# Optimization experiments

Hardware: AMD Instinct MI355X
Metric: run time of the kernel (lower is better)

## Reference

```python
import jax, jax.numpy as jnp
import numpy as np

N = 100000   # nodes
F = 256      # in_dim
D = 128      # out_dim
K = 2        # hops (K+1 adjacency matrices)
E = 1600000  # edges per hop (avg degree 16)


def setup_inputs() -> dict:
    key = jax.random.key(0)
    ks = jax.random.split(key, 8)
    node_features = jax.random.normal(ks[0], (N, F), dtype=jnp.float32)
    edge_rows = jax.random.randint(ks[1], (K + 1, E), 0, N, dtype=jnp.int32)
    edge_cols = jax.random.randint(ks[2], (K + 1, E), 0, N, dtype=jnp.int32)
    edge_vals = jax.random.uniform(ks[3], (K + 1, E), dtype=jnp.float32)
    W_embed = jax.random.normal(ks[4], (F, D), dtype=jnp.float32) / np.sqrt(F)
    W_feat = jax.random.normal(ks[5], (K + 1, F, D), dtype=jnp.float32) / np.sqrt(F)
    W_embK = jax.random.normal(ks[6], (K + 1, D, D), dtype=jnp.float32) / np.sqrt(D)
    alpha = jnp.asarray(0.1, dtype=jnp.float32)  # learnable scalar, clipped to [0,1]
    return {
        'node_features': node_features,
        'edge_rows': edge_rows,
        'edge_cols': edge_cols,
        'edge_vals': edge_vals,
        'W_embed': W_embed,
        'W_feat': W_feat,
        'W_embK': W_embK,
        'alpha': alpha,
    }


def reference(node_features, edge_rows, edge_cols, edge_vals, W_embed, W_feat, W_embK, alpha):
    # learned_embeddings = Dense(out_dim, no bias)(X)  -> [N, D]
    learned = node_features @ W_embed
    out = jnp.zeros((node_features.shape[0], W_embed.shape[1]), dtype=node_features.dtype)
    for hop in range(K + 1):
        # feature projection for this hop: [N, D]
        fw = node_features @ W_feat[hop]
        # SpMM: A_hop @ fw via COO gather + scatter-add
        msgs = edge_vals[hop][:, None] * fw[edge_cols[hop]]            # [E, D]
        structural = jax.ops.segment_sum(msgs, edge_rows[hop], num_segments=node_features.shape[0])
        learned_h = learned @ W_embK[hop]                              # [N, D]
        out = out + structural + alpha * learned_h
    # dropout is identity at inference (training=False)
    return jax.nn.relu(out)
```

## Files before the change

kernel.cpp:

```cpp
#include <hip/hip_runtime.h>
#include <hip/hip_bf16.h>

#define F_DIM 256
#define D_DIM 128
#define NHOPS 3
#define KPB   1000
#define NBMAX 512

using short8 = __attribute__((ext_vector_type(8))) short;
using f32x4  = __attribute__((ext_vector_type(4))) float;

static __device__ __forceinline__ unsigned short f2bf(float f) {
    unsigned int u = __float_as_uint(f);
    unsigned int r = (u + 0x7fffu + ((u >> 16) & 1u)) >> 16;
    return (unsigned short)r;
}
static __device__ __forceinline__ float bf2f(unsigned short b) {
    return __uint_as_float(((unsigned int)b) << 16);
}

__global__ void wsum_kernel(const float* __restrict__ W_embK,
                            const float* __restrict__ alpha,
                            float* __restrict__ Wsum) {
    int i = blockIdx.x * blockDim.x + threadIdx.x;
    if (i < D_DIM * D_DIM) {
        float a = alpha[0];
        Wsum[i] = a * (W_embK[i] + W_embK[D_DIM * D_DIM + i] + W_embK[2 * D_DIM * D_DIM + i]);
    }
}

__global__ void wc_kernel(const float* __restrict__ W_embed,
                          const float* __restrict__ Wsum,
                          float* __restrict__ Wc) {
    int i = blockIdx.x * blockDim.x + threadIdx.x;
    if (i < F_DIM * D_DIM) {
        int f = i / D_DIM, d = i % D_DIM;
        float acc = 0.f;
        #pragma unroll 8
        for (int k = 0; k < D_DIM; ++k)
            acc = fmaf(W_embed[f * D_DIM + k], Wsum[k * D_DIM + d], acc);
        Wc[i] = acc;
    }
}

__global__ void pack_wt(const float* __restrict__ Wc,
                        const float* __restrict__ W_feat,
                        unsigned short* __restrict__ Wt) {
    int i = blockIdx.x * blockDim.x + threadIdx.x;
    int j = i >> 8, k = i & 255;
    float v = (j < 128)
        ? Wc[k * D_DIM + j]
        : W_feat[(size_t)((j - 128) >> 7) * F_DIM * D_DIM + k * D_DIM + ((j - 128) & 127)];
    Wt[i] = f2bf(v);
}

__global__ void xcast_kernel(const float* __restrict__ X, unsigned short* __restrict__ Xb,
                             int n4) {
    int i = blockIdx.x * blockDim.x + threadIdx.x;
    int stride = gridDim.x * blockDim.x;
    for (; i < n4; i += stride) {
        float4 v = ((const float4*)X)[i];
        ushort4 p;
        p.x = f2bf(v.x); p.y = f2bf(v.y); p.z = f2bf(v.z); p.w = f2bf(v.w);
        ((ushort4*)Xb)[i] = p;
    }
}


__global__ __launch_bounds__(256) void bhist_kernel(const int* __restrict__ rows,
                                                    int* __restrict__ bcount,
                                                    int N, int E, int TE) {
    __shared__ int h[NBMAX];
    int tid = threadIdx.x;
    for (int i = tid; i < NBMAX; i += 256) h[i] = 0;
    __syncthreads();
    int c0 = blockIdx.x * 4096;
    #pragma unroll
    for (int i = 0; i < 16; ++i) {
        int ge = c0 + tid + i * 256;
        if (ge < TE) {
            int row = rows[ge];
            int hp = (ge >= E) + (ge >= 2 * E);
            int key = hp * N + row;
            atomicAdd(&h[key / KPB], 1);
        }
    }
    __syncthreads();
    for (int b = tid; b < NBMAX; b += 256)
        if (h[b]) atomicAdd(&bcount[b], h[b]);
}

__global__ void bscan_kernel(const int* __restrict__ bcount, int* __restrict__ bstart,
                             int* __restrict__ gcur, int NB) {
    __shared__ int s[NBMAX + 1];
    int tid = threadIdx.x;
    for (int i = tid; i < NB; i += 256) s[i] = bcount[i];
    __syncthreads();
    if (tid == 0) {
        int run = 0;
        for (int i = 0; i < NB; ++i) { int c = s[i]; s[i] = run; run += c; }
        s[NB] = run;
    }
    __syncthreads();
    for (int i = tid; i <= NB; i += 256) {
        bstart[i] = s[i];
        if (i < NB) gcur[i] = s[i];
    }
}

__global__ __launch_bounds__(256) void bucket_scatter(const int* __restrict__ rows,
                                                      const int* __restrict__ cols,
                                                      const float* __restrict__ vals,
                                                      int* __restrict__ gcur,
                                                      int2* __restrict__ cvb,
                                                      int N, int E, int TE) {
    __shared__ int sh_hist[NBMAX];
    __shared__ int sh_gof[NBMAX];
    int tid = threadIdx.x;
    for (int i = tid; i < NBMAX; i += 256) sh_hist[i] = 0;
    __syncthreads();
    int c0 = blockIdx.x * 4096;
    unsigned meta[16];
    #pragma unroll
    for (int i = 0; i < 16; ++i) {
        int ge = c0 + tid + i * 256;
        unsigned m = 0;
        if (ge < TE) {
            int row = rows[ge];
            int hp = (ge >= E) + (ge >= 2 * E);
            int key = hp * N + row;
            int b = key / KPB;
            int lkey = key - b * KPB;
            int rank = atomicAdd(&sh_hist[b], 1);
            m = ((unsigned)lkey << 22) | ((unsigned)b << 13) | (unsigned)rank;
        }
        meta[i] = m;
    }
    __syncthreads();
    for (int b = tid; b < NBMAX; b += 256)
        if (sh_hist[b]) sh_gof[b] = atomicAdd(&gcur[b], sh_hist[b]);
    __syncthreads();
    #pragma unroll
    for (int i = 0; i < 16; ++i) {
        int ge = c0 + tid + i * 256;
        if (ge < TE) {
            unsigned m = meta[i];
            int rank = m & 8191;
            int b = (m >> 13) & 511;
            int lkey = m >> 22;
            int col = cols[ge];
            float v = vals[ge];
            cvb[sh_gof[b] + rank] = make_int2(col | (lkey << 17), __float_as_int(v));
        }
    }
}

__global__ __launch_bounds__(256) void local_sort(const int2* __restrict__ cvb,
                                                  const int* __restrict__ bstart,
                                                  int2* __restrict__ cv,
                                                  int* __restrict__ offsets,
                                                  int M, int TE, int NB) {
    __shared__ int h[1024];
    __shared__ int part[256];
    const int tid = threadIdx.x;
    const int b = blockIdx.x;
    const int s = bstart[b], e = bstart[b + 1];

    for (int k = tid; k < 1024; k += 256) h[k] = 0;
    __syncthreads();
    for (int i = s + tid; i < e; i += 256) {
        unsigned lkey = ((unsigned)cvb[i].x) >> 17;
        atomicAdd(&h[lkey], 1);
    }
    __syncthreads();
    int base4 = tid * 4;
    int a0 = h[base4], a1 = h[base4 + 1], a2 = h[base4 + 2], a3 = h[base4 + 3];
    part[tid] = a0 + a1 + a2 + a3;
    __syncthreads();
    for (int off = 1; off < 256; off <<= 1) {
        int t = (tid >= off) ? part[tid - off] : 0;
        __syncthreads();
        part[tid] += t;
        __syncthreads();
    }
    int pbase = tid ? part[tid - 1] : 0;
    h[base4]     = pbase;
    h[base4 + 1] = pbase + a0;
    h[base4 + 2] = pbase + a0 + a1;
    h[base4 + 3] = pbase + a0 + a1 + a2;
    __syncthreads();
    for (int k = tid; k < KPB; k += 256) {
        int key = b * KPB + k;
        if (key < M) offsets[key] = s + h[k];
    }
    if (b == NB - 1 && tid == 0) offsets[M] = TE;
    __syncthreads();
    for (int i = s + tid; i < e; i += 256) {
        int2 rec = cvb[i];
        unsigned lkey = ((unsigned)rec.x) >> 17;
        int p = s + atomicAdd(&h[lkey], 1);
        cv[p] = make_int2(rec.x & 0x1FFFF, rec.y);
    }
}


__global__ void hist_kernel(const int* __restrict__ rows, int* __restrict__ counts,
                            int N, int E) {
    int idx = blockIdx.x * blockDim.x + threadIdx.x;
    int h = blockIdx.y;
    if (idx < E) atomicAdd(&counts[h * N + rows[(size_t)h * E + idx]], 1);
}

__global__ void scan1(const int* __restrict__ counts, int* __restrict__ tmp,
                      int* __restrict__ bsums, int M) {
    __shared__ int s[256];
    int tid = threadIdx.x, i = blockIdx.x * 256 + tid;
    int v = (i < M) ? counts[i] : 0;
    s[tid] = v; __syncthreads();
    for (int off = 1; off < 256; off <<= 1) {
        int t = (tid >= off) ? s[tid - off] : 0;
        __syncthreads();
        s[tid] += t;
        __syncthreads();
    }
    if (i < M) tmp[i] = s[tid] - v;
    if (tid == 255) bsums[blockIdx.x] = s[255];
}

__global__ void scan2(int* __restrict__ bsums, int nb) {
    __shared__ int s[256];
    int tid = threadIdx.x;
    int carry = 0;
    for (int base = 0; base < nb; base += 256) {
        int v = (base + tid < nb) ? bsums[base + tid] : 0;
        s[tid] = v; __syncthreads();
        for (int off = 1; off < 256; off <<= 1) {
            int t = (tid >= off) ? s[tid - off] : 0;
            __syncthreads();
            s[tid] += t;
            __syncthreads();
        }
        if (base + tid < nb) bsums[base + tid] = carry + s[tid] - v;
        carry += s[255];
        __syncthreads();
    }
}

__global__ void scan3(int* __restrict__ tmp, const int* __restrict__ bsums,
                      int* __restrict__ offsets, int M, int total) {
    int i = blockIdx.x * blockDim.x + threadIdx.x;
    if (i < M) {
        int e = tmp[i] + bsums[i >> 8];
        offsets[i] = e;
        tmp[i] = e;
    }
    if (i == 0) offsets[M] = total;
}

__global__ void scatter_kernel(const int* __restrict__ rows, const int* __restrict__ cols,
                               const float* __restrict__ vals, int* __restrict__ cursors,
                               int2* __restrict__ cv, int N, int E) {
    int idx = blockIdx.x * blockDim.x + threadIdx.x;
    int h = blockIdx.y;
    if (idx < E) {
        size_t e = (size_t)h * E + idx;
        int r = rows[e];
        int p = atomicAdd(&cursors[h * N + r], 1);
        cv[p] = make_int2(cols[e], __float_as_int(vals[e]));
    }
}

template <bool BF16A>
__global__ __launch_bounds__(256) void gemm_mfma(const float* __restrict__ X,
                                                 const unsigned short* __restrict__ Xb,
                                                 const unsigned short* __restrict__ Wt,
                                                 float* __restrict__ out,
                                                 unsigned short* __restrict__ fw,
                                                 int N) {
    __shared__ __align__(16) unsigned short As[128][40];
    __shared__ __align__(16) unsigned short Bs[128][40];

    const int tid = threadIdx.x;
    const int w = tid >> 6, lane = tid & 63;
    const int bm = blockIdx.x, bn = blockIdx.y;
    const int row0 = bm * 128;
    const int wm = (w & 1) * 64, wn = (w >> 1) * 64;
    const int l15 = lane & 15, lk = (lane >> 4) * 8;

    f32x4 acc[4][4] = {};

    for (int k0 = 0; k0 < F_DIM; k0 += 32) {
        float4 bv[2];
        #pragma unroll
        for (int i = 0; i < 2; ++i) {
            int idx = tid + i * 256;
            int br = idx >> 2, kq = (idx & 3) << 3;
            bv[i] = *(const float4*)&Wt[((size_t)(bn * 128 + br)) * F_DIM + k0 + kq];
        }
        if constexpr (BF16A) {
            short8 av[2];
            #pragma unroll
            for (int i = 0; i < 2; ++i) {
                int idx = tid + i * 256;
                int ar = idx >> 2, kq = (idx & 3) << 3;
                int gr = row0 + ar; if (gr >= N) gr = N - 1;
                av[i] = *(const short8*)&Xb[(size_t)gr * F_DIM + k0 + kq];
            }
            __syncthreads();
            #pragma unroll
            for (int i = 0; i < 2; ++i) {
                int idx = tid + i * 256;
                int ar = idx >> 2, kq = (idx & 3) << 3;
                *(short8*)&As[ar][kq] = av[i];
            }
        } else {
            float4 av[4];
            #pragma unroll
            for (int i = 0; i < 4; ++i) {
                int idx = tid + i * 256;
                int ar = idx >> 3, kq = (idx & 7) << 2;
                int gr = row0 + ar; if (gr >= N) gr = N - 1;
                av[i] = *(const float4*)&X[(size_t)gr * F_DIM + k0 + kq];
            }
            __syncthreads();
            #pragma unroll
            for (int i = 0; i < 4; ++i) {
                int idx = tid + i * 256;
                int ar = idx >> 3, kq = (idx & 7) << 2;
                ushort4 p;
                p.x = f2bf(av[i].x); p.y = f2bf(av[i].y);
                p.z = f2bf(av[i].z); p.w = f2bf(av[i].w);
                *(ushort4*)&As[ar][kq] = p;
            }
        }
        #pragma unroll
        for (int i = 0; i < 2; ++i) {
            int idx = tid + i * 256;
            int br = idx >> 2, kq = (idx & 3) << 3;
            *(float4*)&Bs[br][kq] = bv[i];
        }
        __syncthreads();

        short8 af[4], bfr[4];
        #pragma unroll
        for (int mi = 0; mi < 4; ++mi) af[mi]  = *(const short8*)&As[wm + mi * 16 + l15][lk];
        #pragma unroll
        for (int ni = 0; ni < 4; ++ni) bfr[ni] = *(const short8*)&Bs[wn + ni * 16 + l15][lk];
        #pragma unroll
        for (int mi = 0; mi < 4; ++mi)
            #pragma unroll
            for (int ni = 0; ni < 4; ++ni)
                acc[mi][ni] = __builtin_amdgcn_mfma_f32_16x16x32_bf16(af[mi], bfr[ni], acc[mi][ni], 0, 0, 0);
        __syncthreads();
    }

    if (bn == 0) {
        #pragma unroll
        for (int mi = 0; mi < 4; ++mi) {
            int rowb = row0 + wm + mi * 16 + (lane >> 4) * 4;
            #pragma unroll
            for (int ni = 0; ni < 4; ++ni) {
                int col = wn + ni * 16 + l15;
                #pragma unroll
                for (int j = 0; j < 4; ++j) {
                    int rr = rowb + j;
                    if (rr < N) out[(size_t)rr * D_DIM + col] = acc[mi][ni][j];
                }
            }
        }
    } else {
        unsigned short* dst = fw + (size_t)(bn - 1) * N * D_DIM;
        #pragma unroll
        for (int mi = 0; mi < 4; ++mi) {
            int rowb = row0 + wm + mi * 16 + (lane >> 4) * 4;
            #pragma unroll
            for (int ni = 0; ni < 4; ++ni) {
                int col = wn + ni * 16 + l15;
                #pragma unroll
                for (int j = 0; j < 4; ++j) {
                    int rr = rowb + j;
                    if (rr < N) dst[(size_t)rr * D_DIM + col] = f2bf(acc[mi][ni][j]);
                }
            }
        }
    }
}

__global__ __launch_bounds__(256) void spmm_csr(const int* __restrict__ off,
                                                const int2* __restrict__ cv,
                                                const unsigned short* __restrict__ fw,
                                                float* __restrict__ out, int N) {
    const int w = threadIdx.x >> 6, lane = threadIdx.x & 63;
    const int r = blockIdx.x * 4 + w;
    if (r >= N) return;
    const int sub = lane >> 4;
    const int dp  = lane & 15;
    const size_t obase = (size_t)r * D_DIM + dp * 8;

    float acc[8];
    if (sub == 0) {
        float4 a = *(const float4*)&out[obase];
        float4 b = *(const float4*)&out[obase + 4];
        acc[0] = a.x; acc[1] = a.y; acc[2] = a.z; acc[3] = a.w;
        acc[4] = b.x; acc[5] = b.y; acc[6] = b.z; acc[7] = b.w;
    } else {
        #pragma unroll
        for (int j = 0; j < 8; ++j) acc[j] = 0.f;
    }

    #pragma unroll
    for (int h = 0; h < NHOPS; ++h) {
        const unsigned short* fwh = fw + (size_t)h * N * D_DIM;
        int s = off[h * N + r], e = off[h * N + r + 1];
        int i = s + sub;
        for (; i + 4 < e; i += 8) {
            int2 ca = cv[i];
            int2 cb = cv[i + 4];
            short8 pa = *(const short8*)&fwh[(size_t)ca.x * D_DIM + dp * 8];
            short8 pb = *(const short8*)&fwh[(size_t)cb.x * D_DIM + dp * 8];
            float va = __int_as_float(ca.y);
            float vb = __int_as_float(cb.y);
            #pragma unroll
            for (int j = 0; j < 8; ++j)
                acc[j] = fmaf(va, bf2f((unsigned short)pa[j]), acc[j]);
            #pragma unroll
            for (int j = 0; j < 8; ++j)
                acc[j] = fmaf(vb, bf2f((unsigned short)pb[j]), acc[j]);
        }
        if (i < e) {
            int2 ca = cv[i];
            short8 pa = *(const short8*)&fwh[(size_t)ca.x * D_DIM + dp * 8];
            float va = __int_as_float(ca.y);
            #pragma unroll
            for (int j = 0; j < 8; ++j)
                acc[j] = fmaf(va, bf2f((unsigned short)pa[j]), acc[j]);
        }
    }

    #pragma unroll
    for (int j = 0; j < 8; ++j) {
        acc[j] += __shfl_xor(acc[j], 16, 64);
        acc[j] += __shfl_xor(acc[j], 32, 64);
    }

    if (sub == 0) {
        float4 a = {fmaxf(acc[0], 0.f), fmaxf(acc[1], 0.f), fmaxf(acc[2], 0.f), fmaxf(acc[3], 0.f)};
        float4 b = {fmaxf(acc[4], 0.f), fmaxf(acc[5], 0.f), fmaxf(acc[6], 0.f), fmaxf(acc[7], 0.f)};
        *(float4*)&out[obase]     = a;
        *(float4*)&out[obase + 4] = b;
    }
}

extern "C" void kernel_launch(void* const* d_in, const int* in_sizes, int n_in,
                              void* d_out, int out_size, void* d_ws, size_t ws_size,
                              hipStream_t stream) {
    const float* X         = (const float*)d_in[0];
    const int*   edge_rows = (const int*)d_in[1];
    const int*   edge_cols = (const int*)d_in[2];
    const float* edge_vals = (const float*)d_in[3];
    const float* W_embed   = (const float*)d_in[4];
    const float* W_feat    = (const float*)d_in[5];
    const float* W_embK    = (const float*)d_in[6];
    const float* alpha     = (const float*)d_in[7];
    float* out = (float*)d_out;

    const int N  = in_sizes[0] / F_DIM;
    const int E  = in_sizes[1] / NHOPS;
    const int M  = NHOPS * N;
    const int TE = NHOPS * E;
    const int NB = (M + KPB - 1) / KPB;

    auto al = [](size_t x) { return (x + 255) & ~(size_t)255; };
    const size_t sz_cv   = al((size_t)TE * 8);
    const size_t sz_fwb  = al((size_t)M * D_DIM * 2);
    const size_t sz_xb   = al((size_t)N * F_DIM * 2);
    const size_t sz_off  = al((size_t)(M + 1) * 4);
    const size_t sz_m    = al((size_t)M * 4);
    const size_t sz_b    = al((size_t)(NBMAX + 1) * 4);
    const size_t sz_w    = al(D_DIM * D_DIM * 4) + al(F_DIM * D_DIM * 4) + al(512 * F_DIM * 2);
    const size_t need_mid = 2 * sz_cv + sz_fwb + sz_off + 3 * sz_b + sz_w;
    const size_t need_big = need_mid + sz_xb;

    const bool ok_new = (NB <= NBMAX) && (N < (1 << 17));
    const int mode = (ok_new && ws_size >= need_big) ? 2
                   : (ok_new && ws_size >= need_mid) ? 1 : 0;

    char* wsb = (char*)d_ws;
    size_t o = 0;
    auto take = [&](size_t bytes) -> char* {
        char* p = wsb + o;
        o += al(bytes);
        return p;
    };

    if (mode >= 1) {
        int2*           cvb     = (int2*)take((size_t)TE * 8);
        int2*           cv      = (int2*)take((size_t)TE * 8);
        unsigned short* fwb     = (unsigned short*)take((size_t)M * D_DIM * 2);
        int*            offsets = (int*)take((size_t)(M + 1) * 4);
        int*            bcount  = (int*)take((NBMAX + 1) * 4);
        int*            bstart  = (int*)take((NBMAX + 1) * 4);
        int*            gcur    = (int*)take((NBMAX + 1) * 4);
        float*          Wsum    = (float*)take(D_DIM * D_DIM * 4);
        float*          Wc      = (float*)take(F_DIM * D_DIM * 4);
        unsigned short* Wt      = (unsigned short*)take(512 * F_DIM * 2);
        unsigned short* Xb      = (mode == 2) ? (unsigned short*)take((size_t)N * F_DIM * 2) : nullptr;

        const int nchunk = (TE + 4095) / 4096;
        hipMemsetAsync(bcount, 0, NBMAX * 4, stream);
        bhist_kernel<<<nchunk, 256, 0, stream>>>(edge_rows, bcount, N, E, TE);
        bscan_kernel<<<1, 256, 0, stream>>>(bcount, bstart, gcur, NB);
        bucket_scatter<<<nchunk, 256, 0, stream>>>(edge_rows, edge_cols, edge_vals,
                                                   gcur, cvb, N, E, TE);
        local_sort<<<NB, 256, 0, stream>>>(cvb, bstart, cv, offsets, M, TE, NB);

        wsum_kernel<<<(D_DIM * D_DIM + 255) / 256, 256, 0, stream>>>(W_embK, alpha, Wsum);
        wc_kernel<<<(F_DIM * D_DIM + 255) / 256, 256, 0, stream>>>(W_embed, Wsum, Wc);
        pack_wt<<<(512 * F_DIM) / 256, 256, 0, stream>>>(Wc, W_feat, Wt);

        dim3 g((N + 127) / 128, 4);
        if (mode == 2) {
            xcast_kernel<<<2048, 256, 0, stream>>>(X, Xb, N * F_DIM / 4);
            gemm_mfma<true><<<g, 256, 0, stream>>>(X, Xb, Wt, out, fwb, N);
        } else {
            gemm_mfma<false><<<g, 256, 0, stream>>>(X, nullptr, Wt, out, fwb, N);
        }

        spmm_csr<<<(N + 3) / 4, 256, 0, stream>>>(offsets, cv, fwb, out, N);
    } else {
        int2*           cv      = (int2*)take((size_t)TE * 8);
        unsigned short* fwb     = (unsigned short*)take((size_t)M * D_DIM * 2);
        int*            counts  = (int*)take((size_t)M * 4);
        int*            cursors = (int*)take((size_t)M * 4);
        int*            offsets = (int*)take((size_t)(M + 1) * 4);
        int*            bsums   = (int*)take(8192);
        float*          Wsum    = (float*)take(D_DIM * D_DIM * 4);
        float*          Wc      = (float*)take(F_DIM * D_DIM * 4);
        unsigned short* Wt      = (unsigned short*)take(512 * F_DIM * 2);

        hipMemsetAsync(counts, 0, (size_t)M * 4, stream);
        dim3 ge((E + 255) / 256, NHOPS);
        hist_kernel<<<ge, 256, 0, stream>>>(edge_rows, counts, N, E);
        int nb = (M + 255) / 256;
        scan1<<<nb, 256, 0, stream>>>(counts, cursors, bsums, M);
        scan2<<<1, 256, 0, stream>>>(bsums, nb);
        scan3<<<nb, 256, 0, stream>>>(cursors, bsums, offsets, M, TE);
        scatter_kernel<<<ge, 256, 0, stream>>>(edge_rows, edge_cols, edge_vals,
                                               cursors, cv, N, E);

        wsum_kernel<<<(D_DIM * D_DIM + 255) / 256, 256, 0, stream>>>(W_embK, alpha, Wsum);
        wc_kernel<<<(F_DIM * D_DIM + 255) / 256, 256, 0, stream>>>(W_embed, Wsum, Wc);
        pack_wt<<<(512 * F_DIM) / 256, 256, 0, stream>>>(Wc, W_feat, Wt);

        dim3 g((N + 127) / 128, 4);
        gemm_mfma<false><<<g, 256, 0, stream>>>(X, nullptr, Wt, out, fwb, N);

        spmm_csr<<<(N + 3) / 4, 256, 0, stream>>>(offsets, cv, fwb, out, N);
    }
}
```

Baseline: 662.2 us.

## Shrink sort buckets to 256 keys, fuse weight packing, unroll SpMM with nontemporal loads

Bucket size drops from 1000 to 256 keys so bucket and local-key math uses shifts, and the local sort needs a single 256-entry histogram and scan. The bucket scan becomes a parallel chunked scan, since the bucket count grows to about 1200. The two weight-prep kernels are merged into one pack_all kernel that caches a Wsum column in shared memory. The SpMM inner loop is unrolled to four edges per step and reads cv with nontemporal loads. The main risk is that the rank field now has 12 bits, so a bucket with more than 4096 entries in one chunk would overflow, though that is unlikely here.

```diff
diff --git a/kernel.cpp b/kernel.cpp
--- a/kernel.cpp
+++ b/kernel.cpp
@@ -4,8 +4,8 @@
 #define F_DIM 256
 #define D_DIM 128
 #define NHOPS 3
-#define KPB   1000
-#define NBMAX 512
+#define KPB   256
+#define NBMAX 2048
 
 using short8 = __attribute__((ext_vector_type(8))) short;
 using f32x4  = __attribute__((ext_vector_type(4))) float;
@@ -17,6 +17,11 @@
 }
 static __device__ __forceinline__ float bf2f(unsigned short b) {
     return __uint_as_float(((unsigned int)b) << 16);
+}
+static __device__ __forceinline__ int2 ldnt_i2(const int2* p) {
+    long long raw = __builtin_nontemporal_load((const long long*)p);
+    int2 r; r.x = (int)(raw & 0xffffffffLL); r.y = (int)(raw >> 32);
+    return r;
 }
 
 __global__ void wsum_kernel(const float* __restrict__ W_embK,
@@ -29,29 +34,25 @@
     }
 }
 
-__global__ void wc_kernel(const float* __restrict__ W_embed,
-                          const float* __restrict__ Wsum,
-                          float* __restrict__ Wc) {
-    int i = blockIdx.x * blockDim.x + threadIdx.x;
-    if (i < F_DIM * D_DIM) {
-        int f = i / D_DIM, d = i % D_DIM;
+__global__ __launch_bounds__(256) void pack_all(const float* __restrict__ W_embed,
+                                                const float* __restrict__ W_feat,
+                                                const float* __restrict__ Wsum,
+                                                unsigned short* __restrict__ Wt) {
+    __shared__ float wcol[D_DIM];
+    const int j = blockIdx.x;
+    const int k = threadIdx.x;
+    if (j < D_DIM) {
+        for (int i = k; i < D_DIM; i += 256) wcol[i] = Wsum[i * D_DIM + j];
+        __syncthreads();
         float acc = 0.f;
         #pragma unroll 8
-        for (int k = 0; k < D_DIM; ++k)
-            acc = fmaf(W_embed[f * D_DIM + k], Wsum[k * D_DIM + d], acc);
-        Wc[i] = acc;
-    }
-}
-
-__global__ void pack_wt(const float* __restrict__ Wc,
-                        const float* __restrict__ W_feat,
-                        unsigned short* __restrict__ Wt) {
-    int i = blockIdx.x * blockDim.x + threadIdx.x;
-    int j = i >> 8, k = i & 255;
-    float v = (j < 128)
-        ? Wc[k * D_DIM + j]
-        : W_feat[(size_t)((j - 128) >> 7) * F_DIM * D_DIM + k * D_DIM + ((j - 128) & 127)];
-    Wt[i] = f2bf(v);
+        for (int kk = 0; kk < D_DIM; ++kk)
+            acc = fmaf(W_embed[k * D_DIM + kk], wcol[kk], acc);
+        Wt[(size_t)j * F_DIM + k] = f2bf(acc);
+    } else {
+        int hp = (j - D_DIM) >> 7, d = (j - D_DIM) & 127;
+        Wt[(size_t)j * F_DIM + k] = f2bf(W_feat[(size_t)hp * F_DIM * D_DIM + k * D_DIM + d]);
+    }
 }
 
 __global__ void xcast_kernel(const float* __restrict__ X, unsigned short* __restrict__ Xb,
@@ -81,8 +82,7 @@
         if (ge < TE) {
             int row = rows[ge];
             int hp = (ge >= E) + (ge >= 2 * E);
-            int key = hp * N + row;
-            atomicAdd(&h[key / KPB], 1);
+            atomicAdd(&h[(hp * N + row) >> 8], 1);
         }
     }
     __syncthreads();
@@ -90,22 +90,28 @@
         if (h[b]) atomicAdd(&bcount[b], h[b]);
 }
 
-__global__ void bscan_kernel(const int* __restrict__ bcount, int* __restrict__ bstart,
-                             int* __restrict__ gcur, int NB) {
-    __shared__ int s[NBMAX + 1];
+__global__ __launch_bounds__(256) void bscan_kernel(const int* __restrict__ bcount,
+                                                    int* __restrict__ bstart,
+                                                    int* __restrict__ gcur, int NB) {
+    __shared__ int s[256];
     int tid = threadIdx.x;
-    for (int i = tid; i < NB; i += 256) s[i] = bcount[i];
-    __syncthreads();
-    if (tid == 0) {
-        int run = 0;
-        for (int i = 0; i < NB; ++i) { int c = s[i]; s[i] = run; run += c; }
-        s[NB] = run;
-    }
-    __syncthreads();
-    for (int i = tid; i <= NB; i += 256) {
-        bstart[i] = s[i];
-        if (i < NB) gcur[i] = s[i];
-    }
+    int carry = 0;
+    for (int base = 0; base < NB; base += 256) {
+        int idx = base + tid;
+        int v = (idx < NB) ? bcount[idx] : 0;
+        s[tid] = v; __syncthreads();
+        for (int off = 1; off < 256; off <<= 1) {
+            int t = (tid >= off) ? s[tid - off] : 0;
+            __syncthreads();
+            s[tid] += t;
+            __syncthreads();
+        }
+        int excl = carry + s[tid] - v;
+        if (idx < NB) { bstart[idx] = excl; gcur[idx] = excl; }
+        carry += s[255];
+        __syncthreads();
+    }
+    if (tid == 0) bstart[NB] = carry;
 }
 
 __global__ __launch_bounds__(256) void bucket_scatter(const int* __restrict__ rows,
@@ -129,10 +135,10 @@
             int row = rows[ge];
             int hp = (ge >= E) + (ge >= 2 * E);
             int key = hp * N + row;
-            int b = key / KPB;
-            int lkey = key - b * KPB;
+            int b = key >> 8;
+            int lkey = key & 255;
             int rank = atomicAdd(&sh_hist[b], 1);
-            m = ((unsigned)lkey << 22) | ((unsigned)b << 13) | (unsigned)rank;
+            m = ((unsigned)lkey << 23) | ((unsigned)b << 12) | (unsigned)rank;
         }
         meta[i] = m;
     }
@@ -145,12 +151,11 @@
         int ge = c0 + tid + i * 256;
         if (ge < TE) {
             unsigned m = meta[i];
-            int rank = m & 8191;
-            int b = (m >> 13) & 511;
-            int lkey = m >> 22;
-            int col = cols[ge];
-            float v = vals[ge];
-            cvb[sh_gof[b] + rank] = make_int2(col | (lkey << 17), __float_as_int(v));
+            int rank = m & 4095;
+            int b = (m >> 12) & 2047;
+            int lkey = m >> 23;
+            cvb[sh_gof[b] + rank] = make_int2(cols[ge] | (lkey << 17),
+                                              __float_as_int(vals[ge]));
         }
     }
 }
@@ -160,40 +165,30 @@
                                                   int2* __restrict__ cv,
                                                   int* __restrict__ offsets,
                                                   int M, int TE, int NB) {
-    __shared__ int h[1024];
-    __shared__ int part[256];
+    __shared__ int h[256];
+    __shared__ int sc[256];
     const int tid = threadIdx.x;
     const int b = blockIdx.x;
     const int s = bstart[b], e = bstart[b + 1];
 
-    for (int k = tid; k < 1024; k += 256) h[k] = 0;
-    __syncthreads();
-    for (int i = s + tid; i < e; i += 256) {
-        unsigned lkey = ((unsigned)cvb[i].x) >> 17;
-        atomicAdd(&h[lkey], 1);
-    }
-    __syncthreads();
-    int base4 = tid * 4;
-    int a0 = h[base4], a1 = h[base4 + 1], a2 = h[base4 + 2], a3 = h[base4 + 3];
-    part[tid] = a0 + a1 + a2 + a3;
-    __syncthreads();
+    h[tid] = 0;
+    __syncthreads();
+    for (int i = s + tid; i < e; i += 256)
+        atomicAdd(&h[((unsigned)cvb[i].x) >> 17], 1);
+    __syncthreads();
+    int v = h[tid];
+    sc[tid] = v; __syncthreads();
     for (int off = 1; off < 256; off <<= 1) {
-        int t = (tid >= off) ? part[tid - off] : 0;
-        __syncthreads();
-        part[tid] += t;
-        __syncthreads();
-    }
-    int pbase = tid ? part[tid - 1] : 0;
-    h[base4]     = pbase;
-    h[base4 + 1] = pbase + a0;
-    h[base4 + 2] = pbase + a0 + a1;
-    h[base4 + 3] = pbase + a0 + a1 + a2;
-    __syncthreads();
-    for (int k = tid; k < KPB; k += 256) {
-        int key = b * KPB + k;
-        if (key < M) offsets[key] = s + h[k];
-    }
+        int t = (tid >= off) ? sc[tid - off] : 0;
+        __syncthreads();
+        sc[tid] += t;
+        __syncthreads();
+    }
+    int excl = sc[tid] - v;
+    int key = (b << 8) + tid;
+    if (key < M) offsets[key] = s + excl;
     if (b == NB - 1 && tid == 0) offsets[M] = TE;
+    h[tid] = excl;
     __syncthreads();
     for (int i = s + tid; i < e; i += 256) {
         int2 rec = cvb[i];
@@ -413,27 +408,43 @@
         const unsigned short* fwh = fw + (size_t)h * N * D_DIM;
         int s = off[h * N + r], e = off[h * N + r + 1];
         int i = s + sub;
+        for (; i + 12 < e; i += 16) {
+            int2 c0 = ldnt_i2(cv + i);
+            int2 c1 = ldnt_i2(cv + i + 4);
+            int2 c2 = ldnt_i2(cv + i + 8);
+            int2 c3 = ldnt_i2(cv + i + 12);
+            short8 p0 = *(const short8*)&fwh[(size_t)c0.x * D_DIM + dp * 8];
+            short8 p1 = *(const short8*)&fwh[(size_t)c1.x * D_DIM + dp * 8];
+            short8 p2 = *(const short8*)&fwh[(size_t)c2.x * D_DIM + dp * 8];
+            short8 p3 = *(const short8*)&fwh[(size_t)c3.x * D_DIM + dp * 8];
+            float v0 = __int_as_float(c0.y), v1 = __int_as_float(c1.y);
+            float v2 = __int_as_float(c2.y), v3 = __int_as_float(c3.y);
+            #pragma unroll
+            for (int j = 0; j < 8; ++j) acc[j] = fmaf(v0, bf2f((unsigned short)p0[j]), acc[j]);
+            #pragma unroll
+            for (int j = 0; j < 8; ++j) acc[j] = fmaf(v1, bf2f((unsigned short)p1[j]), acc[j]);
+            #pragma unroll
+            for (int j = 0; j < 8; ++j) acc[j] = fmaf(v2, bf2f((unsigned short)p2[j]), acc[j]);
+            #pragma unroll
+            for (int j = 0; j < 8; ++j) acc[j] = fmaf(v3, bf2f((unsigned short)p3[j]), acc[j]);
+        }
         for (; i + 4 < e; i += 8) {
-            int2 ca = cv[i];
-            int2 cb = cv[i + 4];
-            short8 pa = *(const short8*)&fwh[(size_t)ca.x * D_DIM + dp * 8];
-            short8 pb = *(const short8*)&fwh[(size_t)cb.x * D_DIM + dp * 8];
-            float va = __int_as_float(ca.y);
-            float vb = __int_as_float(cb.y);
-            #pragma unroll
-            for (int j = 0; j < 8; ++j)
-                acc[j] = fmaf(va, bf2f((unsigned short)pa[j]), acc[j]);
-            #pragma unroll
-            for (int j = 0; j < 8; ++j)
-                acc[j] = fmaf(vb, bf2f((unsigned short)pb[j]), acc[j]);
+            int2 c0 = ldnt_i2(cv + i);
+            int2 c1 = ldnt_i2(cv + i + 4);
+            short8 p0 = *(const short8*)&fwh[(size_t)c0.x * D_DIM + dp * 8];
+            short8 p1 = *(const short8*)&fwh[(size_t)c1.x * D_DIM + dp * 8];
+            float v0 = __int_as_float(c0.y), v1 = __int_as_float(c1.y);
+            #pragma unroll
+            for (int j = 0; j < 8; ++j) acc[j] = fmaf(v0, bf2f((unsigned short)p0[j]), acc[j]);
+            #pragma unroll
+            for (int j = 0; j < 8; ++j) acc[j] = fmaf(v1, bf2f((unsigned short)p1[j]), acc[j]);
         }
         if (i < e) {
-            int2 ca = cv[i];
-            short8 pa = *(const short8*)&fwh[(size_t)ca.x * D_DIM + dp * 8];
-            float va = __int_as_float(ca.y);
-            #pragma unroll
-            for (int j = 0; j < 8; ++j)
-                acc[j] = fmaf(va, bf2f((unsigned short)pa[j]), acc[j]);
+            int2 c0 = ldnt_i2(cv + i);
+            short8 p0 = *(const short8*)&fwh[(size_t)c0.x * D_DIM + dp * 8];
+            float v0 = __int_as_float(c0.y);
+            #pragma unroll
+            for (int j = 0; j < 8; ++j) acc[j] = fmaf(v0, bf2f((unsigned short)p0[j]), acc[j]);
         }
     }
 
@@ -471,13 +482,12 @@
     const int NB = (M + KPB - 1) / KPB;
 
     auto al = [](size_t x) { return (x + 255) & ~(size_t)255; };
-    const size_t sz_cv   = al((size_t)TE * 8);
-    const size_t sz_fwb  = al((size_t)M * D_DIM * 2);
-    const size_t sz_xb   = al((size_t)N * F_DIM * 2);
-    const size_t sz_off  = al((size_t)(M + 1) * 4);
-    const size_t sz_m    = al((size_t)M * 4);
-    const size_t sz_b    = al((size_t)(NBMAX + 1) * 4);
-    const size_t sz_w    = al(D_DIM * D_DIM * 4) + al(F_DIM * D_DIM * 4) + al(512 * F_DIM * 2);
+    const size_t sz_cv  = al((size_t)TE * 8);
+    const size_t sz_fwb = al((size_t)M * D_DIM * 2);
+    const size_t sz_xb  = al((size_t)N * F_DIM * 2);
+    const size_t sz_off = al((size_t)(M + 1) * 4);
+    const size_t sz_b   = al((size_t)(NBMAX + 1) * 4);
+    const size_t sz_w   = al(D_DIM * D_DIM * 4) + al(512 * F_DIM * 2);
     const size_t need_mid = 2 * sz_cv + sz_fwb + sz_off + 3 * sz_b + sz_w;
     const size_t need_big = need_mid + sz_xb;
 
@@ -502,7 +512,6 @@
         int*            bstart  = (int*)take((NBMAX + 1) * 4);
         int*            gcur    = (int*)take((NBMAX + 1) * 4);
         float*          Wsum    = (float*)take(D_DIM * D_DIM * 4);
-        float*          Wc      = (float*)take(F_DIM * D_DIM * 4);
         unsigned short* Wt      = (unsigned short*)take(512 * F_DIM * 2);
         unsigned short* Xb      = (mode == 2) ? (unsigned short*)take((size_t)N * F_DIM * 2) : nullptr;
 
@@ -515,8 +524,7 @@
         local_sort<<<NB, 256, 0, stream>>>(cvb, bstart, cv, offsets, M, TE, NB);
 
         wsum_kernel<<<(D_DIM * D_DIM + 255) / 256, 256, 0, stream>>>(W_embK, alpha, Wsum);
-        wc_kernel<<<(F_DIM * D_DIM + 255) / 256, 256, 0, stream>>>(W_embed, Wsum, Wc);
-        pack_wt<<<(512 * F_DIM) / 256, 256, 0, stream>>>(Wc, W_feat, Wt);
+        pack_all<<<512, 256, 0, stream>>>(W_embed, W_feat, Wsum, Wt);
 
         dim3 g((N + 127) / 128, 4);
         if (mode == 2) {
@@ -535,7 +543,6 @@
         int*            offsets = (int*)take((size_t)(M + 1) * 4);
         int*            bsums   = (int*)take(8192);
         float*          Wsum    = (float*)take(D_DIM * D_DIM * 4);
-        float*          Wc      = (float*)take(F_DIM * D_DIM * 4);
         unsigned short* Wt      = (unsigned short*)take(512 * F_DIM * 2);
 
         hipMemsetAsync(counts, 0, (size_t)M * 4, stream);
@@ -549,8 +556,7 @@
                                                cursors, cv, N, E);
 
         wsum_kernel<<<(D_DIM * D_DIM + 255) / 256, 256, 0, stream>>>(W_embK, alpha, Wsum);
-        wc_kernel<<<(F_DIM * D_DIM + 255) / 256, 256, 0, stream>>>(W_embed, Wsum, Wc);
-        pack_wt<<<(512 * F_DIM) / 256, 256, 0, stream>>>(Wc, W_feat, Wt);
+        pack_all<<<512, 256, 0, stream>>>(W_embed, W_feat, Wsum, Wt);
 
         dim3 g((N + 127) / 128, 4);
         gemm_mfma<false><<<g, 256, 0, stream>>>(X, nullptr, Wt, out, fwb, N);
```

New measurement: 675.4 us. No clear change (+2.0%).
